# Kernel tuning notes

Measured on AMD Instinct MI355X. Metric: run time of the kernel, lower is better.

## Reference

```python
import jax, jax.numpy as jnp
import numpy as np

HW = 256  # fixed UV/image resolution hardcoded in the module


def _grid_sample_nearest(inp, grid):
    """torch.F.grid_sample(mode='nearest', padding_mode='zeros', align_corners=False).
    inp: [N,C,H,W], grid: [N,Hg,Wg,2] with (x,y) in [-1,1]. Returns [N,C,Hg,Wg]."""
    N, C, H, W = inp.shape
    x = grid[..., 0]
    y = grid[..., 1]
    # align_corners=False pixel mapping
    ix = jnp.round(((x + 1.0) * W - 1.0) * 0.5).astype(jnp.int32)
    iy = jnp.round(((y + 1.0) * H - 1.0) * 0.5).astype(jnp.int32)
    valid = (ix >= 0) & (ix < W) & (iy >= 0) & (iy < H)
    ixc = jnp.clip(ix, 0, W - 1)
    iyc = jnp.clip(iy, 0, H - 1)
    gathered = jax.vmap(lambda im, yy, xx: im[:, yy, xx])(inp, iyc, ixc)  # [N,C,Hg,Wg]
    return gathered * valid[:, None, :, :].astype(inp.dtype)


def setup_inputs() -> dict:
    key = jax.random.key(0)
    k1, k2, k3, k4 = jax.random.split(key, 4)
    bs = 128
    grid = jax.random.uniform(k1, (bs, 2, HW, HW), jnp.float32, -1.0, 1.0)
    seg = jax.random.uniform(k2, (bs, 1, HW, HW), jnp.float32)
    conf_is = jax.random.uniform(k3, (bs, 1, HW, HW), jnp.float32)
    depth = jax.random.normal(k4, (bs, 1, HW, HW), jnp.float32)
    return {"grid": grid, "seg": seg, "conf_is": conf_is, "depth": depth}


def reference(grid, seg, conf_is, depth):
    bs = grid.shape[0]
    # segmentation mask with all-True fallback for empty masks
    seg_mask = seg > 0.5  # [bs,1,H,W] bool
    n_valid = jnp.sum(seg_mask, axis=(1, 2, 3))
    seg_mask = jnp.where((n_valid == 0)[:, None, None, None], True, seg_mask)

    gridm = grid * seg_mask  # bool broadcast over channel dim
    grid_int = ((gridm + 1.0) * 0.5 * HW).astype(jnp.int32)  # trunc-toward-zero == torch .long()
    grid_int = jnp.clip(grid_int, 0, HW - 1)

    # meshgrid_uv[h, w] = [w, h]
    hh, ww = jnp.meshgrid(jnp.arange(HW), jnp.arange(HW), indexing='ij')
    mesh_uv = jnp.stack([ww, hh], axis=-1).astype(jnp.float32)  # [H,W,2]

    # per-batch scatter write: grid_uv[b, gy, gx] = mesh_uv  (the irregular-access hot spot)
    def scatter_one(gy, gx):
        return jnp.zeros((HW, HW, 2), jnp.float32).at[gy, gx].set(mesh_uv)

    grid_uv = jax.vmap(scatter_one)(grid_int[:, 1], grid_int[:, 0])  # [bs,H,W,2]
    grid_uv = grid_uv / 128.0 - 1.0

    mesh_x = jnp.broadcast_to((ww / 280.0).astype(jnp.float32)[None, None], (bs, 1, HW, HW))
    mesh_y = jnp.broadcast_to((hh / 280.0).astype(jnp.float32)[None, None], (bs, 1, HW, HW))
    dkpt_img = jnp.concatenate([mesh_x, mesh_y, depth], axis=1) * seg_mask  # [bs,3,H,W]

    dkpt_uv = _grid_sample_nearest(dkpt_img, grid_uv)           # [bs,3,H,W]
    conf_is_uv = _grid_sample_nearest(conf_is, grid_uv)          # [bs,1,H,W]
    mask_uv = _grid_sample_nearest(seg_mask.astype(jnp.float32), grid_uv)[:, 0]  # [bs,H,W]
    return dkpt_uv, conf_is_uv, mask_uv
```

## Files before the change

kernel.cpp:

```cpp
#include <hip/hip_runtime.h>

#define HW    256
#define HW2   65536
#define BS    128
#define NTS   1024
#define QPB   16384
#define HQ    8192


__device__ __forceinline__ void lds_max_u16(unsigned int* W32, int cell, unsigned int val) {
    unsigned int* word = W32 + (cell >> 1);
    unsigned int sh = (cell & 1) << 4;
    unsigned int assumed = *word;
    while (((assumed >> sh) & 0xFFFFu) < val) {
        unsigned int nw = (assumed & ~(0xFFFFu << sh)) | (val << sh);
        unsigned int prev = atomicCAS(word, assumed, nw);
        if (prev == assumed) break;
        assumed = prev;
    }
}

__global__ __launch_bounds__(NTS, 1) void scatter_kernel(
        const float* __restrict__ grid,
        const float* __restrict__ seg,
        const float* __restrict__ conf,
        const float* __restrict__ depth,
        unsigned short* __restrict__ W16,
        float4* __restrict__ packed) {
    __shared__ unsigned short Wl[HW2];
    __shared__ int red[16];
    __shared__ int flag_s;

    const int b    = blockIdx.x & (BS - 1);
    const int h    = blockIdx.x >> 7;
    const int tid  = threadIdx.x;
    const int wave = tid >> 6;
    const int lane = tid & 63;
    unsigned int* W32 = (unsigned int*)Wl;

    const float* segb   = seg   + (size_t)b * HW2;
    const float* confb  = conf  + (size_t)b * HW2;
    const float* depthb = depth + (size_t)b * HW2;

    {
        uint4* Wz = (uint4*)W32;
        #pragma unroll
        for (int k = 0; k < 8; ++k) Wz[tid + k * NTS] = make_uint4(0u, 0u, 0u, 0u);
    }
    unsigned int mbits = 0u;
    int cnt = 0;
    {
        const float4* s4 = (const float4*)segb;
        #pragma unroll
        for (int k = 0; k < 8; ++k) {
            float4 v = s4[h * HQ + tid + k * NTS];
            unsigned q = (v.x > 0.5f ? 1u : 0u) | (v.y > 0.5f ? 2u : 0u) |
                         (v.z > 0.5f ? 4u : 0u) | (v.w > 0.5f ? 8u : 0u);
            mbits |= q << (k * 4);
            cnt += __popc(q);
        }
        #pragma unroll
        for (int k = 0; k < 8; ++k) {
            float4 v = s4[(1 - h) * HQ + tid + k * NTS];
            cnt += (v.x > 0.5f) + (v.y > 0.5f) + (v.z > 0.5f) + (v.w > 0.5f);
        }
    }
    for (int off = 32; off > 0; off >>= 1) cnt += __shfl_down(cnt, off);
    if (lane == 0) red[wave] = cnt;
    __syncthreads();
    if (tid == 0) {
        int t = 0;
        #pragma unroll
        for (int w = 0; w < 16; ++w) t += red[w];
        flag_s = (t == 0) ? 1 : 0;
    }
    __syncthreads();
    const int flagb = flag_s;

    {
        const float4* gx4 = (const float4*)(grid + (size_t)(2 * b) * HW2);
        const float4* gy4 = (const float4*)(grid + (size_t)(2 * b + 1) * HW2);
        int masked_max = -1;
        #pragma unroll 4
        for (int k = 0; k < 8; ++k) {
            int i = h * HQ + tid + k * NTS;
            float4 X = gx4[i];
            float4 Y = gy4[i];
            int hw0 = i * 4;
            float xa[4] = {X.x, X.y, X.z, X.w};
            float ya[4] = {Y.x, Y.y, Y.z, Y.w};
            #pragma unroll
            for (int j = 0; j < 4; ++j) {
                bool m = flagb || ((mbits >> (k * 4 + j)) & 1u);
                if (m) {
                    float fx = (xa[j] + 1.0f) * 0.5f * 256.0f;
                    float fy = (ya[j] + 1.0f) * 0.5f * 256.0f;
                    int gxi = min(max((int)fx, 0), HW - 1);
                    int gyi = min(max((int)fy, 0), HW - 1);
                    lds_max_u16(W32, gyi * HW + gxi, (unsigned int)(hw0 + j));
                } else {
                    masked_max = hw0 + j;
                }
            }
        }
        int mm = masked_max;
        for (int off = 32; off > 0; off >>= 1) mm = max(mm, __shfl_xor(mm, off));
        if (lane == 0 && mm >= 0)
            lds_max_u16(W32, 128 * HW + 128, (unsigned int)mm);
    }

    {
        float4* packb = packed + (size_t)b * 16384;
        #pragma unroll
        for (int rr = 0; rr < 4; ++rr) {
            int rl = wave * 4 + rr;
            int r  = 128 * h + 2 * rl;
            int qr = r * 64 + lane;
            float4 d = ((const float4*)depthb)[qr];
            float4 c = ((const float4*)confb)[qr];
            float4 s = ((const float4*)segb)[qr];
            float m0 = (flagb || s.x > 0.5f) ? 1.0f : 0.0f;
            float m1 = (flagb || s.z > 0.5f) ? 1.0f : 0.0f;
            int p = (r >> 1) * 128 + 2 * lane;
            packb[p]     = make_float4(d.x * m0, c.x, m0, 0.0f);
            packb[p + 1] = make_float4(d.z * m1, c.z, m1, 0.0f);
        }
    }
    __syncthreads();

    {
        unsigned short* Wout = W16 + ((size_t)h * BS + b) * HW2;
        const uint4* Wl4 = (const uint4*)Wl;
        #pragma unroll
        for (int k = 0; k < 8; ++k)
            ((uint4*)Wout)[tid + k * NTS] = Wl4[tid + k * NTS];
    }
}

__global__ __launch_bounds__(256, 8) void gather_kernel(
        const unsigned short* __restrict__ W16,
        const float4* __restrict__ packed,
        float* __restrict__ out) {
    __shared__ float lut[128];
    if (threadIdx.x < 128) lut[threadIdx.x] = (float)(2 * threadIdx.x) / 280.0f;
    __syncthreads();

    const int B   = blockIdx.x;
    const int xcd = B & 7;
    const int k   = B >> 3;
    const int b   = (k & 15) * 8 + xcd;
    const int s   = k >> 4;
    const int q0  = s * 1024;

    const unsigned short* W0 = W16 + (size_t)b * HW2;
    const unsigned short* W1 = W16 + ((size_t)BS + b) * HW2;
    const float4* packb = packed + (size_t)b * 16384;
    float4* out4 = (float4*)out;
    const size_t dkBase = (size_t)(b * 3) * QPB;
    const size_t O1 = (size_t)BS * 3 * QPB + (size_t)b * QPB;
    const size_t O2 = (size_t)BS * 4 * QPB + (size_t)b * QPB;

    #pragma unroll
    for (int t = 0; t < 4; ++t) {
        int q = q0 + threadIdx.x + t * 256;
        uint2 a  = ((const uint2*)W0)[q];
        uint2 c2 = ((const uint2*)W1)[q];
        unsigned la[4] = { max(a.x & 0xFFFFu, c2.x & 0xFFFFu),
                           max(a.x >> 16,     c2.x >> 16),
                           max(a.y & 0xFFFFu, c2.y & 0xFFFFu),
                           max(a.y >> 16,     c2.y >> 16) };
        float o0[4], o1[4], o2v[4], oc[4], om[4];
        #pragma unroll
        for (int j = 0; j < 4; ++j) {
            unsigned l = la[j];
            int ix = (int)(l & 255u) & ~1;
            int iy = (int)(l >> 8) & ~1;
            float4 p = packb[(iy >> 1) * 128 + (ix >> 1)];
            float m = p.z;
            o0[j]  = lut[ix >> 1] * m;
            o1[j]  = lut[iy >> 1] * m;
            o2v[j] = p.x;
            oc[j]  = p.y;
            om[j]  = m;
        }
        out4[dkBase + q]           = make_float4(o0[0], o0[1], o0[2], o0[3]);
        out4[dkBase + QPB + q]     = make_float4(o1[0], o1[1], o1[2], o1[3]);
        out4[dkBase + 2 * QPB + q] = make_float4(o2v[0], o2v[1], o2v[2], o2v[3]);
        out4[O1 + q]               = make_float4(oc[0], oc[1], oc[2], oc[3]);
        out4[O2 + q]               = make_float4(om[0], om[1], om[2], om[3]);
    }
}

#define NT 1024
#define QQ 4096
__global__ __launch_bounds__(NT, 8) void fused_kernel(
        const float* __restrict__ grid,
        const float* __restrict__ seg,
        const float* __restrict__ conf,
        const float* __restrict__ depth,
        float* __restrict__ out) {
    __shared__ unsigned int Wl[HW2 / 4];
    __shared__ unsigned long long segbits[4][256];
    __shared__ int red[16];
    __shared__ int flag_s;
    const int b       = blockIdx.x & (BS - 1);
    const int quarter = blockIdx.x >> 7;
    const int tid  = threadIdx.x;
    const int wave = tid >> 6;
    const int lane = tid & 63;
    const float* segb   = seg   + (size_t)b * HW2;
    const float* confb  = conf  + (size_t)b * HW2;
    const float* depthb = depth + (size_t)b * HW2;
    {
        uint4* Wz = (uint4*)Wl;
        #pragma unroll
        for (int k = 0; k < 4; ++k) Wz[tid + k * NT] = make_uint4(0u, 0u, 0u, 0u);
    }
    unsigned long long mbits = 0ULL;
    int cnt = 0;
    {
        const float4* s4 = (const float4*)segb;
        #pragma unroll
        for (int k = 0; k < 16; ++k) {
            int i = tid + k * NT;
            float4 v = s4[i];
            bool px = v.x > 0.5f, py = v.y > 0.5f, pz = v.z > 0.5f, pw = v.w > 0.5f;
            unsigned long long bx = __ballot(px), by = __ballot(py);
            unsigned long long bz = __ballot(pz), bw = __ballot(pw);
            if (lane == 0) {
                int wi = wave + k * 16;
                segbits[0][wi] = bx; segbits[1][wi] = by;
                segbits[2][wi] = bz; segbits[3][wi] = bw;
                cnt += __popcll(bx) + __popcll(by) + __popcll(bz) + __popcll(bw);
            }
            unsigned long long q = (px ? 1ULL : 0ULL) | (py ? 2ULL : 0ULL) |
                                   (pz ? 4ULL : 0ULL) | (pw ? 8ULL : 0ULL);
            mbits |= q << (k * 4);
        }
    }
    if (lane == 0) red[wave] = cnt;
    __syncthreads();
    if (tid == 0) {
        int t = 0;
        #pragma unroll
        for (int w = 0; w < 16; ++w) t += red[w];
        flag_s = (t == 0) ? 1 : 0;
    }
    __syncthreads();
    const int flagb = flag_s;
    {
        const float4* gx4 = (const float4*)(grid + (size_t)(2 * b) * HW2);
        const float4* gy4 = (const float4*)(grid + (size_t)(2 * b + 1) * HW2);
        int masked_max = -1;
        #pragma unroll 4
        for (int k = 0; k < 16; ++k) {
            int i = tid + k * NT;
            float4 X = gx4[i];
            float4 Y = gy4[i];
            int hw0 = i * 4;
            float xa[4] = {X.x, X.y, X.z, X.w};
            float ya[4] = {Y.x, Y.y, Y.z, Y.w};
            #pragma unroll
            for (int j = 0; j < 4; ++j) {
                bool m = flagb || ((mbits >> (k * 4 + j)) & 1ULL);
                if (m) {
                    float fx = (xa[j] + 1.0f) * 0.5f * 256.0f;
                    float fy = (ya[j] + 1.0f) * 0.5f * 256.0f;
                    int gxi = min(max((int)fx, 0), HW - 1);
                    int gyi = min(max((int)fy, 0), HW - 1);
                    if ((gyi >> 6) == quarter)
                        atomicMax(&Wl[(gyi & 63) * HW + gxi], (unsigned int)(hw0 + j));
                } else {
                    masked_max = hw0 + j;
                }
            }
        }
        int mm = masked_max;
        for (int off = 32; off > 0; off >>= 1) mm = max(mm, __shfl_xor(mm, off));
        if (quarter == 2 && lane == 0 && mm >= 0)
            atomicMax(&Wl[(128 & 63) * HW + 128], (unsigned int)mm);
    }
    __syncthreads();
    float4* out4 = (float4*)out;
    const size_t dkBase = (size_t)(b * 3) * QPB;
    const size_t O1q = (size_t)BS * 3 * QPB + (size_t)b * QPB;
    const size_t O2q = (size_t)BS * 4 * QPB + (size_t)b * QPB;
    #pragma unroll 4
    for (int k = 0; k < 4; ++k) {
        int i = tid + k * NT;
        uint4 wv = ((const uint4*)Wl)[i];
        unsigned la[4] = {wv.x, wv.y, wv.z, wv.w};
        float o0[4], o1[4], o2[4], oc[4], om[4];
        #pragma unroll
        for (int j = 0; j < 4; ++j) {
            unsigned l = la[j];
            int ix = (int)(l & 255u) & ~1;
            int iy = (int)(l >> 8) & ~1;
            int off = iy * HW + ix;
            int q = off >> 2;
            float m;
            if (flagb) m = 1.0f;
            else       m = (float)((segbits[off & 3][q >> 6] >> (q & 63)) & 1ULL);
            o0[j] = ((float)ix / 280.0f) * m;
            o1[j] = ((float)iy / 280.0f) * m;
            o2[j] = depthb[off] * m;
            oc[j] = confb[off];
            om[j] = m;
        }
        size_t gq = (size_t)quarter * QQ + i;
        out4[dkBase + gq]           = make_float4(o0[0], o0[1], o0[2], o0[3]);
        out4[dkBase + QPB + gq]     = make_float4(o1[0], o1[1], o1[2], o1[3]);
        out4[dkBase + 2 * QPB + gq] = make_float4(o2[0], o2[1], o2[2], o2[3]);
        out4[O1q + gq]              = make_float4(oc[0], oc[1], oc[2], oc[3]);
        out4[O2q + gq]              = make_float4(om[0], om[1], om[2], om[3]);
    }
}

extern "C" void kernel_launch(void* const* d_in, const int* in_sizes, int n_in,
                              void* d_out, int out_size, void* d_ws, size_t ws_size,
                              hipStream_t stream) {
    const float* grid  = (const float*)d_in[0];
    const float* seg   = (const float*)d_in[1];
    const float* conf  = (const float*)d_in[2];
    const float* depth = (const float*)d_in[3];
    float* out = (float*)d_out;

    const size_t W16Bytes  = (size_t)2 * BS * HW2 * sizeof(unsigned short);
    const size_t packBytes = (size_t)BS * 16384 * sizeof(float4);
    if (ws_size >= W16Bytes + packBytes) {
        unsigned short* W16 = (unsigned short*)d_ws;
        float4* packed = (float4*)((char*)d_ws + W16Bytes);
        scatter_kernel<<<BS * 2, NTS, 0, stream>>>(grid, seg, conf, depth, W16, packed);
        gather_kernel<<<2048, 256, 0, stream>>>(W16, packed, out);
    } else {
        fused_kernel<<<BS * 4, NT, 0, stream>>>(grid, seg, conf, depth, out);
    }
}
```

Before: 329.8 us.

## Partition scatter by destination row quarter with native LDS atomicMax

The scatter kernel now splits each batch by destination-row quarter instead of source half. Every block reads all grid points but only writes the 64 destination rows it owns, using a 32-bit LDS table with native atomicMax in place of a 16-bit CAS loop. Each block then packs its table to 16-bit in the workspace, so the gather kernel reads one table per batch and no longer needs a max-merge of two partial tables. The cost is that every block reads the full grid and seg data (4x redundant input reads), in exchange for cheaper atomics, more blocks and smaller LDS use per block.

```diff
diff --git a/kernel.cpp b/kernel.cpp
--- a/kernel.cpp
+++ b/kernel.cpp
@@ -3,66 +3,47 @@
 #define HW    256
 #define HW2   65536
 #define BS    128
-#define NTS   1024
+#define NT    1024
 #define QPB   16384
-#define HQ    8192
-
-
-__device__ __forceinline__ void lds_max_u16(unsigned int* W32, int cell, unsigned int val) {
-    unsigned int* word = W32 + (cell >> 1);
-    unsigned int sh = (cell & 1) << 4;
-    unsigned int assumed = *word;
-    while (((assumed >> sh) & 0xFFFFu) < val) {
-        unsigned int nw = (assumed & ~(0xFFFFu << sh)) | (val << sh);
-        unsigned int prev = atomicCAS(word, assumed, nw);
-        if (prev == assumed) break;
-        assumed = prev;
-    }
-}
-
-__global__ __launch_bounds__(NTS, 1) void scatter_kernel(
+
+
+__global__ __launch_bounds__(NT, 8) void scatter_kernel(
         const float* __restrict__ grid,
         const float* __restrict__ seg,
         const float* __restrict__ conf,
         const float* __restrict__ depth,
         unsigned short* __restrict__ W16,
         float4* __restrict__ packed) {
-    __shared__ unsigned short Wl[HW2];
+    __shared__ unsigned int Wl[HW2 / 4];
     __shared__ int red[16];
     __shared__ int flag_s;
 
     const int b    = blockIdx.x & (BS - 1);
-    const int h    = blockIdx.x >> 7;
+    const int q    = blockIdx.x >> 7;
     const int tid  = threadIdx.x;
     const int wave = tid >> 6;
     const int lane = tid & 63;
-    unsigned int* W32 = (unsigned int*)Wl;
 
     const float* segb   = seg   + (size_t)b * HW2;
     const float* confb  = conf  + (size_t)b * HW2;
     const float* depthb = depth + (size_t)b * HW2;
 
     {
-        uint4* Wz = (uint4*)W32;
-        #pragma unroll
-        for (int k = 0; k < 8; ++k) Wz[tid + k * NTS] = make_uint4(0u, 0u, 0u, 0u);
-    }
-    unsigned int mbits = 0u;
+        uint4* Wz = (uint4*)Wl;
+        #pragma unroll
+        for (int k = 0; k < 4; ++k) Wz[tid + k * NT] = make_uint4(0u, 0u, 0u, 0u);
+    }
+    unsigned long long mbits = 0ULL;
     int cnt = 0;
     {
         const float4* s4 = (const float4*)segb;
         #pragma unroll
-        for (int k = 0; k < 8; ++k) {
-            float4 v = s4[h * HQ + tid + k * NTS];
-            unsigned q = (v.x > 0.5f ? 1u : 0u) | (v.y > 0.5f ? 2u : 0u) |
-                         (v.z > 0.5f ? 4u : 0u) | (v.w > 0.5f ? 8u : 0u);
-            mbits |= q << (k * 4);
-            cnt += __popc(q);
-        }
-        #pragma unroll
-        for (int k = 0; k < 8; ++k) {
-            float4 v = s4[(1 - h) * HQ + tid + k * NTS];
-            cnt += (v.x > 0.5f) + (v.y > 0.5f) + (v.z > 0.5f) + (v.w > 0.5f);
+        for (int k = 0; k < 16; ++k) {
+            float4 v = s4[tid + k * NT];
+            unsigned long long qm = (v.x > 0.5f ? 1ULL : 0ULL) | (v.y > 0.5f ? 2ULL : 0ULL) |
+                                    (v.z > 0.5f ? 4ULL : 0ULL) | (v.w > 0.5f ? 8ULL : 0ULL);
+            mbits |= qm << (k * 4);
+            cnt += __popcll(qm);
         }
     }
     for (int off = 32; off > 0; off >>= 1) cnt += __shfl_down(cnt, off);
@@ -82,8 +63,8 @@
         const float4* gy4 = (const float4*)(grid + (size_t)(2 * b + 1) * HW2);
         int masked_max = -1;
         #pragma unroll 4
-        for (int k = 0; k < 8; ++k) {
-            int i = h * HQ + tid + k * NTS;
+        for (int k = 0; k < 16; ++k) {
+            int i = tid + k * NT;
             float4 X = gx4[i];
             float4 Y = gy4[i];
             int hw0 = i * 4;
@@ -91,13 +72,14 @@
             float ya[4] = {Y.x, Y.y, Y.z, Y.w};
             #pragma unroll
             for (int j = 0; j < 4; ++j) {
-                bool m = flagb || ((mbits >> (k * 4 + j)) & 1u);
+                bool m = flagb || ((mbits >> (k * 4 + j)) & 1ULL);
                 if (m) {
                     float fx = (xa[j] + 1.0f) * 0.5f * 256.0f;
                     float fy = (ya[j] + 1.0f) * 0.5f * 256.0f;
                     int gxi = min(max((int)fx, 0), HW - 1);
                     int gyi = min(max((int)fy, 0), HW - 1);
-                    lds_max_u16(W32, gyi * HW + gxi, (unsigned int)(hw0 + j));
+                    if ((gyi >> 6) == q)
+                        atomicMax(&Wl[(gyi & 63) * HW + gxi], (unsigned int)(hw0 + j));
                 } else {
                     masked_max = hw0 + j;
                 }
@@ -105,35 +87,44 @@
         }
         int mm = masked_max;
         for (int off = 32; off > 0; off >>= 1) mm = max(mm, __shfl_xor(mm, off));
-        if (lane == 0 && mm >= 0)
-            lds_max_u16(W32, 128 * HW + 128, (unsigned int)mm);
+        if (q == 2 && lane == 0 && mm >= 0)
+            atomicMax(&Wl[(128 & 63) * HW + 128], (unsigned int)mm);
+    }
+    __syncthreads();
+
+    {
+        unsigned int* Wout = (unsigned int*)(W16 + (size_t)b * HW2 + q * 16384);
+        #pragma unroll
+        for (int k = 0; k < 2; ++k) {
+            int idx = tid + k * NT;
+            int base = idx * 8;
+            uint4 w;
+            w.x = Wl[base + 0] | (Wl[base + 1] << 16);
+            w.y = Wl[base + 2] | (Wl[base + 3] << 16);
+            w.z = Wl[base + 4] | (Wl[base + 5] << 16);
+            w.w = Wl[base + 6] | (Wl[base + 7] << 16);
+            ((uint4*)Wout)[idx] = w;
+        }
     }
 
     {
         float4* packb = packed + (size_t)b * 16384;
         #pragma unroll
-        for (int rr = 0; rr < 4; ++rr) {
-            int rl = wave * 4 + rr;
-            int r  = 128 * h + 2 * rl;
-            int qr = r * 64 + lane;
+        for (int k = 0; k < 2; ++k) {
+            int it = tid + k * NT;
+            int rl = it >> 6;
+            int qc = it & 63;
+            int r  = 64 * q + 2 * rl;
+            int qr = r * 64 + qc;
             float4 d = ((const float4*)depthb)[qr];
             float4 c = ((const float4*)confb)[qr];
             float4 s = ((const float4*)segb)[qr];
             float m0 = (flagb || s.x > 0.5f) ? 1.0f : 0.0f;
             float m1 = (flagb || s.z > 0.5f) ? 1.0f : 0.0f;
-            int p = (r >> 1) * 128 + 2 * lane;
+            int p = (r >> 1) * 128 + 2 * qc;
             packb[p]     = make_float4(d.x * m0, c.x, m0, 0.0f);
             packb[p + 1] = make_float4(d.z * m1, c.z, m1, 0.0f);
         }
-    }
-    __syncthreads();
-
-    {
-        unsigned short* Wout = W16 + ((size_t)h * BS + b) * HW2;
-        const uint4* Wl4 = (const uint4*)Wl;
-        #pragma unroll
-        for (int k = 0; k < 8; ++k)
-            ((uint4*)Wout)[tid + k * NTS] = Wl4[tid + k * NTS];
     }
 }
 
@@ -153,7 +144,6 @@
     const int q0  = s * 1024;
 
     const unsigned short* W0 = W16 + (size_t)b * HW2;
-    const unsigned short* W1 = W16 + ((size_t)BS + b) * HW2;
     const float4* packb = packed + (size_t)b * 16384;
     float4* out4 = (float4*)out;
     const size_t dkBase = (size_t)(b * 3) * QPB;
@@ -162,13 +152,9 @@
 
     #pragma unroll
     for (int t = 0; t < 4; ++t) {
-        int q = q0 + threadIdx.x + t * 256;
-        uint2 a  = ((const uint2*)W0)[q];
-        uint2 c2 = ((const uint2*)W1)[q];
-        unsigned la[4] = { max(a.x & 0xFFFFu, c2.x & 0xFFFFu),
-                           max(a.x >> 16,     c2.x >> 16),
-                           max(a.y & 0xFFFFu, c2.y & 0xFFFFu),
-                           max(a.y >> 16,     c2.y >> 16) };
+        int qd = q0 + threadIdx.x + t * 256;
+        uint2 a = ((const uint2*)W0)[qd];
+        unsigned la[4] = { a.x & 0xFFFFu, a.x >> 16, a.y & 0xFFFFu, a.y >> 16 };
         float o0[4], o1[4], o2v[4], oc[4], om[4];
         #pragma unroll
         for (int j = 0; j < 4; ++j) {
@@ -183,15 +169,14 @@
             oc[j]  = p.y;
             om[j]  = m;
         }
-        out4[dkBase + q]           = make_float4(o0[0], o0[1], o0[2], o0[3]);
-        out4[dkBase + QPB + q]     = make_float4(o1[0], o1[1], o1[2], o1[3]);
-        out4[dkBase + 2 * QPB + q] = make_float4(o2v[0], o2v[1], o2v[2], o2v[3]);
-        out4[O1 + q]               = make_float4(oc[0], oc[1], oc[2], oc[3]);
-        out4[O2 + q]               = make_float4(om[0], om[1], om[2], om[3]);
+        out4[dkBase + qd]           = make_float4(o0[0], o0[1], o0[2], o0[3]);
+        out4[dkBase + QPB + qd]     = make_float4(o1[0], o1[1], o1[2], o1[3]);
+        out4[dkBase + 2 * QPB + qd] = make_float4(o2v[0], o2v[1], o2v[2], o2v[3]);
+        out4[O1 + qd]               = make_float4(oc[0], oc[1], oc[2], oc[3]);
+        out4[O2 + qd]               = make_float4(om[0], om[1], om[2], om[3]);
     }
 }
 
-#define NT 1024
 #define QQ 4096
 __global__ __launch_bounds__(NT, 8) void fused_kernel(
         const float* __restrict__ grid,
@@ -297,10 +282,10 @@
             int ix = (int)(l & 255u) & ~1;
             int iy = (int)(l >> 8) & ~1;
             int off = iy * HW + ix;
-            int q = off >> 2;
+            int qq = off >> 2;
             float m;
             if (flagb) m = 1.0f;
-            else       m = (float)((segbits[off & 3][q >> 6] >> (q & 63)) & 1ULL);
+            else       m = (float)((segbits[off & 3][qq >> 6] >> (qq & 63)) & 1ULL);
             o0[j] = ((float)ix / 280.0f) * m;
             o1[j] = ((float)iy / 280.0f) * m;
             o2[j] = depthb[off] * m;
@@ -325,12 +310,12 @@
     const float* depth = (const float*)d_in[3];
     float* out = (float*)d_out;
 
-    const size_t W16Bytes  = (size_t)2 * BS * HW2 * sizeof(unsigned short);
+    const size_t W16Bytes  = (size_t)BS * HW2 * sizeof(unsigned short);
     const size_t packBytes = (size_t)BS * 16384 * sizeof(float4);
     if (ws_size >= W16Bytes + packBytes) {
         unsigned short* W16 = (unsigned short*)d_ws;
         float4* packed = (float4*)((char*)d_ws + W16Bytes);
-        scatter_kernel<<<BS * 2, NTS, 0, stream>>>(grid, seg, conf, depth, W16, packed);
+        scatter_kernel<<<BS * 4, NT, 0, stream>>>(grid, seg, conf, depth, W16, packed);
         gather_kernel<<<2048, 256, 0, stream>>>(W16, packed, out);
     } else {
         fused_kernel<<<BS * 4, NT, 0, stream>>>(grid, seg, conf, depth, out);
```

New measurement: 331.2 us. About the same (+0.4%).
